# Performance work log

Measured on AMD Instinct MI355X. Metric: run time of the kernel, lower is better.

## Reference

```python
import jax, jax.numpy as jnp
import numpy as np

B, T, C, H = 4, 4096, 512, 64

def setup_inputs() -> dict:
    key = jax.random.key(0)
    ks = jax.random.split(key, 9)
    k = jax.random.normal(ks[0], (B, T, C), dtype=jnp.float32)
    v = jax.random.normal(ks[1], (B, T, C), dtype=jnp.float32)
    q = jax.random.normal(ks[2], (B, T, C), dtype=jnp.float32)
    # causal lower-triangular mask, positions with 0 are masked to -inf
    mask = jnp.tril(jnp.ones((T, T), dtype=jnp.int32))
    s = 1.0 / np.sqrt(C)
    kW = jax.random.normal(ks[3], (C, H), dtype=jnp.float32) * s
    kb = jax.random.normal(ks[4], (H,), dtype=jnp.float32) * s
    vW = jax.random.normal(ks[5], (C, H), dtype=jnp.float32) * s
    vb = jax.random.normal(ks[6], (H,), dtype=jnp.float32) * s
    qW = jax.random.normal(ks[7], (C, H), dtype=jnp.float32) * s
    qb = jax.random.normal(ks[8], (H,), dtype=jnp.float32) * s
    return {"k": k, "v": v, "q": q, "mask": mask,
            "kW": kW, "kb": kb, "vW": vW, "vb": vb, "qW": qW, "qb": qb}

def reference(k, v, q, mask, kW, kb, vW, vb, qW, qb):
    C_in = k.shape[-1]
    kp = k @ kW + kb                              # [B,T,H]
    qp = q @ qW + qb                              # [B,T,H]
    # NOTE: original scales by embedding_size**-0.5 (C), not head_size**-0.5
    attn = jnp.einsum('bth,bsh->bts', qp, kp) * (C_in ** -0.5)  # [B,T,T]
    attn = jnp.where(mask[None, :, :] == 0, -jnp.inf, attn)
    attn = jax.nn.softmax(attn, axis=-1)
    vp = v @ vW + vb                              # [B,T,H]
    out = attn @ vp                               # [B,T,H]
    return out
```

## Files before the change

### kernel.cpp

```cpp
#include <hip/hip_runtime.h>
#include <hip/hip_bf16.h>

#define Bq 4
#define Tq 4096
#define Cq 512
#define Hq 64
#define NEG_BIG (-3.0e38f)

using bf16   = __bf16;
using bf16x8 = __attribute__((ext_vector_type(8))) __bf16;
using bf16x4 = __attribute__((ext_vector_type(4))) __bf16;
using f32x4  = __attribute__((ext_vector_type(4))) float;
using f32x16 = __attribute__((ext_vector_type(16))) float;

static __device__ __forceinline__ float other_half_f(float x) {
    return __shfl_xor(x, 32, 64);
}
static __device__ __forceinline__ unsigned other_half_u(unsigned x) {
    return (unsigned)__shfl_xor((int)x, 32, 64);
}
static __device__ __forceinline__ unsigned pk2(float x, float y) {
    union { bf16 h[2]; unsigned u; } t;
    t.h[0] = (bf16)x; t.h[1] = (bf16)y;
    return t.u;
}
union W8 { unsigned u[4]; bf16x8 v; };

#define BUILD_B(p, BA, BB) do {                                                \
    const unsigned w0 = pk2(p[0],  p[1]),  w1 = pk2(p[2],  p[3]);              \
    const unsigned w2 = pk2(p[4],  p[5]),  w3 = pk2(p[6],  p[7]);              \
    const unsigned w4 = pk2(p[8],  p[9]),  w5 = pk2(p[10], p[11]);             \
    const unsigned w6 = pk2(p[12], p[13]), w7 = pk2(p[14], p[15]);             \
    const unsigned o0 = other_half_u(w0), o1 = other_half_u(w1);               \
    const unsigned o2 = other_half_u(w2), o3 = other_half_u(w3);               \
    const unsigned o4 = other_half_u(w4), o5 = other_half_u(w5);               \
    const unsigned o6 = other_half_u(w6), o7 = other_half_u(w7);               \
    BA.u[0] = hi ? o2 : w0;  BA.u[1] = hi ? o3 : w1;                           \
    BA.u[2] = hi ? w2 : o0;  BA.u[3] = hi ? w3 : o1;                           \
    BB.u[0] = hi ? o6 : w4;  BB.u[1] = hi ? o7 : w5;                           \
    BB.u[2] = hi ? w6 : o4;  BB.u[3] = hi ? w7 : o5;                           \
} while (0)

__global__ __launch_bounds__(256) void prep_weights_kernel(
    const float* __restrict__ kW, const float* __restrict__ qW,
    const float* __restrict__ vW, bf16* __restrict__ WT)
{
    int i = blockIdx.x * 256 + threadIdx.x;
    int t = i >> 15;
    int r = i & 32767;
    int c = r >> 6;
    int h = r & 63;
    const float* W = (t == 0) ? kW : (t == 1) ? qW : vW;
    WT[(size_t)t * 32768 + h * 512 + c] = (bf16)W[r];
}

__global__ __launch_bounds__(128) void proj_kernel(
    const float* __restrict__ Xk, const float* __restrict__ Xq,
    const float* __restrict__ Xv, const bf16* __restrict__ WT,
    const float* __restrict__ bk, const float* __restrict__ bq,
    const float* __restrict__ bv,
    bf16* __restrict__ kp, bf16* __restrict__ qp, bf16* __restrict__ vpT)
{
    const int t    = blockIdx.y;
    const int lane = threadIdx.x & 63;
    const int wave = threadIdx.x >> 6;
    const int lq   = lane & 15;
    const int lg   = lane >> 4;
    const int row0 = blockIdx.x * 32 + wave * 16;

    const float* X    = (t == 0) ? Xk : (t == 1) ? Xq : Xv;
    const float* bias = (t == 0) ? bk : (t == 1) ? bq : bv;
    const bf16*  Wt   = WT + (size_t)t * (Hq * Cq);

    const float* Xrow = X + (size_t)(row0 + lq) * Cq + lg * 8;

    f32x4 acc[4];
#pragma unroll
    for (int i = 0; i < 4; ++i) acc[i] = f32x4{0.f, 0.f, 0.f, 0.f};

#pragma unroll 4
    for (int kc = 0; kc < Cq; kc += 32) {
        float4 a0 = *(const float4*)(Xrow + kc);
        float4 a1 = *(const float4*)(Xrow + kc + 4);
        bf16x8 af;
        af[0] = (bf16)a0.x; af[1] = (bf16)a0.y; af[2] = (bf16)a0.z; af[3] = (bf16)a0.w;
        af[4] = (bf16)a1.x; af[5] = (bf16)a1.y; af[6] = (bf16)a1.z; af[7] = (bf16)a1.w;
#pragma unroll
        for (int ht = 0; ht < 4; ++ht) {
            bf16x8 bfB = *(const bf16x8*)(Wt + (size_t)(ht * 16 + lq) * Cq + kc + lg * 8);
            acc[ht] = __builtin_amdgcn_mfma_f32_16x16x32_bf16(af, bfB, acc[ht], 0, 0, 0);
        }
    }

    const float scale = (t == 1) ? (0.044194173824159216f * 1.4426950408889634f) : 1.0f;

    if (t < 2) {
        bf16* dst = (t == 0) ? kp : qp;
#pragma unroll
        for (int ht = 0; ht < 4; ++ht) {
            float bb = bias[ht * 16 + lq];
#pragma unroll
            for (int r = 0; r < 4; ++r) {
                int row = row0 + 4 * lg + r;
                dst[(size_t)row * Hq + ht * 16 + lq] = (bf16)((acc[ht][r] + bb) * scale);
            }
        }
    } else {
#pragma unroll
        for (int ht = 0; ht < 4; ++ht) {
            float bb = bias[ht * 16 + lq];
            bf16x4 pk;
#pragma unroll
            for (int r = 0; r < 4; ++r) pk[r] = (bf16)(acc[ht][r] + bb);
            int rowg = row0 + 4 * lg;
            int bidx = rowg >> 12;
            int tt   = rowg & 4095;
            int h    = ht * 16 + lq;
            *(bf16x4*)(vpT + (((size_t)(bidx * Hq + h)) << 12) + tt) = pk;
        }
    }
}

__global__ __launch_bounds__(256, 2) void attn_kernel(
    const bf16* __restrict__ qp, const bf16* __restrict__ kp,
    const bf16* __restrict__ vpT,
    bf16* __restrict__ PO, float* __restrict__ PML)
{
    __shared__ char lds_raw[2][16384];

    const int x = blockIdx.x;
    const int b = x & 3;
    const int j = 31 - ((x >> 2) & 31);
    const int c = x >> 7;
    const int kstart = c * 512;
    const int klim   = (j + 1) * 128;
    if (kstart >= klim) return;
    const int kend = min(kstart + 512, klim);
    const int nt   = (kend - kstart) >> 6;

    const int tid  = threadIdx.x;
    const int wid  = tid >> 6;
    const int lane = tid & 63;
    const int l31  = lane & 31;
    const int half = lane >> 5;
    const bool hi  = half != 0;
    const int qt   = j * 4 + wid;
    const int qb   = qt * 32;
    const int qg   = qb + l31;
    const int qlast = qb + 31;

    const bf16* kp_b = kp  + (size_t)b * Tq * Hq;
    const bf16* vp_b = vpT + (size_t)b * Hq * Tq;

    const int srow = tid >> 2;
    const int sseg = (tid & 3) * 16;
    const int sswz = (srow & 7) << 4;

#define STAGE_LOAD(T, r0, r1, r2, r3) do {                                     \
    const int k0_ = kstart + (T) * 64;                                         \
    const bf16* kg_ = kp_b + (size_t)(k0_ + srow) * Hq + (sseg >> 1);          \
    r0 = *(const int4*)(kg_);                                                  \
    r1 = *(const int4*)(kg_ + 32);                                             \
    const bf16* vg_ = vp_b + (size_t)srow * Tq + k0_ + (sseg >> 1);            \
    r2 = *(const int4*)(vg_);                                                  \
    r3 = *(const int4*)(vg_ + 32);                                             \
} while (0)

#define STAGE_WRITE(BUF, r0, r1, r2, r3) do {                                  \
    char* base_ = lds_raw[BUF];                                                \
    *(int4*)(base_ + srow * 128 + (sseg ^ sswz))          = r0;                \
    *(int4*)(base_ + srow * 128 + ((sseg + 64) ^ sswz))   = r1;                \
    *(int4*)(base_ + 8192 + srow * 128 + (sseg ^ sswz))        = r2;           \
    *(int4*)(base_ + 8192 + srow * 128 + ((sseg + 64) ^ sswz)) = r3;           \
} while (0)

    const bf16* qrow = qp + ((size_t)b * Tq + qb + l31) * Hq + half * 8;
    const bf16x8 Q0 = *(const bf16x8*)(qrow);
    const bf16x8 Q1 = *(const bf16x8*)(qrow + 16);
    const bf16x8 Q2 = *(const bf16x8*)(qrow + 32);
    const bf16x8 Q3 = *(const bf16x8*)(qrow + 48);

    f32x16 O0, O1;
#pragma unroll
    for (int r = 0; r < 16; ++r) { O0[r] = 0.f; O1[r] = 0.f; }
    float l = 0.f;

    const int rswz = (l31 & 7) << 4;
    const int cb   = half * 16;

    int4 s0, s1, s2, s3;
    STAGE_LOAD(0, s0, s1, s2, s3);
    STAGE_WRITE(0, s0, s1, s2, s3);
    __syncthreads();

    int cur = 0;
    for (int t = 0; t < nt; ++t) {
        const bool more = (t + 1 < nt);
        if (more) STAGE_LOAD(t + 1, s0, s1, s2, s3);

        const int k0t = kstart + t * 64;
        if (k0t <= qlast) {
            const char* base = lds_raw[cur];
            const char* kr0 = base + l31 * 128;
            const char* kr1 = base + (32 + l31) * 128;
            const char* vr0 = base + 8192 + l31 * 128;
            const char* vr1 = base + 8192 + (32 + l31) * 128;

            const bf16x8 K00 = *(const bf16x8*)(kr0 + ((cb +  0) ^ rswz));
            const bf16x8 K01 = *(const bf16x8*)(kr0 + ((cb + 32) ^ rswz));
            const bf16x8 K02 = *(const bf16x8*)(kr0 + ((cb + 64) ^ rswz));
            const bf16x8 K03 = *(const bf16x8*)(kr0 + ((cb + 96) ^ rswz));
            const bf16x8 K10 = *(const bf16x8*)(kr1 + ((cb +  0) ^ rswz));
            const bf16x8 K11 = *(const bf16x8*)(kr1 + ((cb + 32) ^ rswz));
            const bf16x8 K12 = *(const bf16x8*)(kr1 + ((cb + 64) ^ rswz));
            const bf16x8 K13 = *(const bf16x8*)(kr1 + ((cb + 96) ^ rswz));
            const bf16x8 Vh0k0 = *(const bf16x8*)(vr0 + ((cb +  0) ^ rswz));
            const bf16x8 Vh0k1 = *(const bf16x8*)(vr0 + ((cb + 32) ^ rswz));
            const bf16x8 Vh0k2 = *(const bf16x8*)(vr0 + ((cb + 64) ^ rswz));
            const bf16x8 Vh0k3 = *(const bf16x8*)(vr0 + ((cb + 96) ^ rswz));
            const bf16x8 Vh1k0 = *(const bf16x8*)(vr1 + ((cb +  0) ^ rswz));
            const bf16x8 Vh1k1 = *(const bf16x8*)(vr1 + ((cb + 32) ^ rswz));
            const bf16x8 Vh1k2 = *(const bf16x8*)(vr1 + ((cb + 64) ^ rswz));
            const bf16x8 Vh1k3 = *(const bf16x8*)(vr1 + ((cb + 96) ^ rswz));

            f32x16 S0, S1;
#pragma unroll
            for (int r = 0; r < 16; ++r) { S0[r] = 0.f; S1[r] = 0.f; }
            S0 = __builtin_amdgcn_mfma_f32_32x32x16_bf16(K00, Q0, S0, 0, 0, 0);
            S1 = __builtin_amdgcn_mfma_f32_32x32x16_bf16(K10, Q0, S1, 0, 0, 0);
            S0 = __builtin_amdgcn_mfma_f32_32x32x16_bf16(K01, Q1, S0, 0, 0, 0);
            S1 = __builtin_amdgcn_mfma_f32_32x32x16_bf16(K11, Q1, S1, 0, 0, 0);
            S0 = __builtin_amdgcn_mfma_f32_32x32x16_bf16(K02, Q2, S0, 0, 0, 0);
            S1 = __builtin_amdgcn_mfma_f32_32x32x16_bf16(K12, Q2, S1, 0, 0, 0);
            S0 = __builtin_amdgcn_mfma_f32_32x32x16_bf16(K03, Q3, S0, 0, 0, 0);
            S1 = __builtin_amdgcn_mfma_f32_32x32x16_bf16(K13, Q3, S1, 0, 0, 0);

            if (k0t + 63 > qb) {
#pragma unroll
                for (int r = 0; r < 16; ++r) {
                    const int kg = k0t + (r & 3) + 8 * (r >> 2) + 4 * half;
                    if (kg > qg)      S0[r] = NEG_BIG;
                    if (kg + 32 > qg) S1[r] = NEG_BIG;
                }
            }

            float p0[16], p1[16];
#pragma unroll
            for (int r = 0; r < 16; ++r) {
                p0[r] = exp2f(S0[r]);
                p1[r] = exp2f(S1[r]);
            }
            l += (((p0[0]+p0[1])+(p0[2]+p0[3])) + ((p0[4]+p0[5])+(p0[6]+p0[7])))
               + (((p0[8]+p0[9])+(p0[10]+p0[11])) + ((p0[12]+p0[13])+(p0[14]+p0[15])))
               + (((p1[0]+p1[1])+(p1[2]+p1[3])) + ((p1[4]+p1[5])+(p1[6]+p1[7])))
               + (((p1[8]+p1[9])+(p1[10]+p1[11])) + ((p1[12]+p1[13])+(p1[14]+p1[15])));

            W8 B00, B01, B10, B11;
            BUILD_B(p0, B00, B01);
            BUILD_B(p1, B10, B11);

            O0 = __builtin_amdgcn_mfma_f32_32x32x16_bf16(Vh0k0, B00.v, O0, 0, 0, 0);
            O1 = __builtin_amdgcn_mfma_f32_32x32x16_bf16(Vh1k0, B00.v, O1, 0, 0, 0);
            O0 = __builtin_amdgcn_mfma_f32_32x32x16_bf16(Vh0k1, B01.v, O0, 0, 0, 0);
            O1 = __builtin_amdgcn_mfma_f32_32x32x16_bf16(Vh1k1, B01.v, O1, 0, 0, 0);
            O0 = __builtin_amdgcn_mfma_f32_32x32x16_bf16(Vh0k2, B10.v, O0, 0, 0, 0);
            O1 = __builtin_amdgcn_mfma_f32_32x32x16_bf16(Vh1k2, B10.v, O1, 0, 0, 0);
            O0 = __builtin_amdgcn_mfma_f32_32x32x16_bf16(Vh0k3, B11.v, O0, 0, 0, 0);
            O1 = __builtin_amdgcn_mfma_f32_32x32x16_bf16(Vh1k3, B11.v, O1, 0, 0, 0);
        }

        __syncthreads();
        if (more) STAGE_WRITE(cur ^ 1, s0, s1, s2, s3);
        __syncthreads();
        cur ^= 1;
    }
#undef STAGE_LOAD
#undef STAGE_WRITE

    const float ltot = l + other_half_f(l);
    const float inv  = (ltot > 0.f) ? (1.0f / ltot) : 0.f;
    const size_t slot = ((size_t)(b * 128 + qt)) * 8 + c;
    bf16* po = PO + slot * 2048;
#pragma unroll
    for (int r = 0; r < 16; ++r) {
        const int h = (r & 3) + 8 * (r >> 2) + 4 * half;
        po[h * 32 + l31]        = (bf16)(O0[r] * inv);
        po[(h + 32) * 32 + l31] = (bf16)(O1[r] * inv);
    }
    if (lane < 32) {
        PML[slot * 32 + l31] = ltot;
    }
}

__global__ __launch_bounds__(256) void combine_kernel(
    const bf16* __restrict__ PO, const float* __restrict__ PML,
    float* __restrict__ out)
{
    const int gid = blockIdx.x;
    const int b   = gid & 3;
    const int qt  = gid >> 2;
    const int qb  = qt * 32;
    const int nch = ((qt >> 2) + 4) >> 2;
    const size_t slot0 = ((size_t)(b * 128 + qt)) * 8;
    const int tid = threadIdx.x;
    const int q   = tid & 31;
    const int hh  = tid >> 5;

    float L = 0.f;
    float acc[8];
#pragma unroll
    for (int i = 0; i < 8; ++i) acc[i] = 0.f;

    for (int c = 0; c < nch; ++c) {
        const float w = PML[(slot0 + c) * 32 + q];
        L += w;
        const bf16* po = PO + (slot0 + c) * 2048;
#pragma unroll
        for (int ih = 0; ih < 8; ++ih)
            acc[ih] += w * (float)po[(hh + 8 * ih) * 32 + q];
    }
    const float inv = 1.0f / L;
#pragma unroll
    for (int ih = 0; ih < 8; ++ih)
        out[((size_t)b * Tq + qb + q) * Hq + hh + 8 * ih] = acc[ih] * inv;
}

extern "C" void kernel_launch(void* const* d_in, const int* in_sizes, int n_in,
                              void* d_out, int out_size, void* d_ws, size_t ws_size,
                              hipStream_t stream)
{
    const float* k  = (const float*)d_in[0];
    const float* v  = (const float*)d_in[1];
    const float* q  = (const float*)d_in[2];
    const float* kW = (const float*)d_in[4];
    const float* kb = (const float*)d_in[5];
    const float* vW = (const float*)d_in[6];
    const float* vb = (const float*)d_in[7];
    const float* qW = (const float*)d_in[8];
    const float* qb = (const float*)d_in[9];
    float* out = (float*)d_out;

    char* ws = (char*)d_ws;
    bf16*  WT  = (bf16*)(ws);
    bf16*  kp  = (bf16*)(ws + 196608);
    bf16*  qp  = (bf16*)(ws + 196608 + 2097152);
    bf16*  vpT = (bf16*)(ws + 196608 + 2 * 2097152);
    bf16*  PO  = (bf16*)(ws + 196608 + 3 * 2097152);
    float* PML = (float*)(ws + 196608 + 3 * 2097152 + 16777216);

    hipLaunchKernelGGL(prep_weights_kernel, dim3(384), dim3(256), 0, stream,
                       kW, qW, vW, WT);
    hipLaunchKernelGGL(proj_kernel, dim3(512, 3), dim3(128), 0, stream,
                       k, q, v, WT, kb, qb, vb, kp, qp, vpT);
    hipLaunchKernelGGL(attn_kernel, dim3(1024), dim3(256), 0, stream,
                       qp, kp, vpT, PO, PML);
    hipLaunchKernelGGL(combine_kernel, dim3(512), dim3(256), 0, stream,
                       PO, PML, out);
}
```

Baseline: 82.67 us.

## Stage projection inputs into LDS via async global_load_lds with swizzled double buffer

The projection kernel now runs one wave per 16-row block. Each block streams its full 16x512 fp32 input tile into LDS as two halves, using direct global-to-LDS 16-byte loads with an XOR swizzle. The first half's MFMA work starts while the second half is still in flight, and row reads are fully coalesced instead of strided 32-byte per-lane reads. The trade-off is 32KB of LDS per single-wave block, which limits how many waves can reside on each CU.

New measurement: 84.43 us. 2.1% more time.

```diff
diff --git a/kernel.cpp b/kernel.cpp
--- a/kernel.cpp
+++ b/kernel.cpp
@@ -54,43 +54,89 @@
     WT[(size_t)t * 32768 + h * 512 + c] = (bf16)W[r];
 }
 
-__global__ __launch_bounds__(128) void proj_kernel(
+__global__ __launch_bounds__(64) void proj_kernel(
     const float* __restrict__ Xk, const float* __restrict__ Xq,
     const float* __restrict__ Xv, const bf16* __restrict__ WT,
     const float* __restrict__ bk, const float* __restrict__ bq,
     const float* __restrict__ bv,
     bf16* __restrict__ kp, bf16* __restrict__ qp, bf16* __restrict__ vpT)
 {
-    const int t    = blockIdx.y;
-    const int lane = threadIdx.x & 63;
-    const int wave = threadIdx.x >> 6;
-    const int lq   = lane & 15;
-    const int lg   = lane >> 4;
-    const int row0 = blockIdx.x * 32 + wave * 16;
-
+    __shared__ float Xs[2][16 * 256];
+
+    const int t = blockIdx.y;
     const float* X    = (t == 0) ? Xk : (t == 1) ? Xq : Xv;
     const float* bias = (t == 0) ? bk : (t == 1) ? bq : bv;
     const bf16*  Wt   = WT + (size_t)t * (Hq * Cq);
 
-    const float* Xrow = X + (size_t)(row0 + lq) * Cq + lg * 8;
+    const int lane = threadIdx.x;
+    const int lq   = lane & 15;
+    const int lg   = lane >> 4;
+    const int row0 = blockIdx.x * 16;
+    const float* Xb = X + (size_t)row0 * Cq;
+
+#define STAGE(BUF, HALF) do {                                                  \
+    _Pragma("unroll")                                                          \
+    for (int i = 0; i < 16; ++i) {                                             \
+        const float* src_ = Xb + (size_t)i * Cq + (HALF) * 256                 \
+                          + ((lane ^ (i & 7)) << 2);                           \
+        __builtin_amdgcn_global_load_lds(                                      \
+            (const __attribute__((address_space(1))) void*)(src_),             \
+            (__attribute__((address_space(3))) void*)(&Xs[BUF][i * 256]),      \
+            16, 0, 0);                                                         \
+    }                                                                          \
+} while (0)
+
+    STAGE(0, 0);
+    __builtin_amdgcn_sched_barrier(0);
+    STAGE(1, 1);
+    __builtin_amdgcn_sched_barrier(0);
 
     f32x4 acc[4];
 #pragma unroll
     for (int i = 0; i < 4; ++i) acc[i] = f32x4{0.f, 0.f, 0.f, 0.f};
 
-#pragma unroll 4
-    for (int kc = 0; kc < Cq; kc += 32) {
-        float4 a0 = *(const float4*)(Xrow + kc);
-        float4 a1 = *(const float4*)(Xrow + kc + 4);
+    const int rx = lq & 7;
+    const float* lrow0 = &Xs[0][lq * 256];
+    const float* lrow1 = &Xs[1][lq * 256];
+
+    asm volatile("s_waitcnt vmcnt(16)" ::: "memory");
+    __builtin_amdgcn_sched_barrier(0);
+
+#pragma unroll
+    for (int st = 0; st < 8; ++st) {
+        const int u0 = st * 8 + lg * 2;
+        const float4 x0 = *(const float4*)(lrow0 + (((u0)     ^ rx) << 2));
+        const float4 x1 = *(const float4*)(lrow0 + (((u0 + 1) ^ rx) << 2));
         bf16x8 af;
-        af[0] = (bf16)a0.x; af[1] = (bf16)a0.y; af[2] = (bf16)a0.z; af[3] = (bf16)a0.w;
-        af[4] = (bf16)a1.x; af[5] = (bf16)a1.y; af[6] = (bf16)a1.z; af[7] = (bf16)a1.w;
+        af[0] = (bf16)x0.x; af[1] = (bf16)x0.y; af[2] = (bf16)x0.z; af[3] = (bf16)x0.w;
+        af[4] = (bf16)x1.x; af[5] = (bf16)x1.y; af[6] = (bf16)x1.z; af[7] = (bf16)x1.w;
+        const int kg = st * 32;
 #pragma unroll
         for (int ht = 0; ht < 4; ++ht) {
-            bf16x8 bfB = *(const bf16x8*)(Wt + (size_t)(ht * 16 + lq) * Cq + kc + lg * 8);
+            bf16x8 bfB = *(const bf16x8*)(Wt + (size_t)(ht * 16 + lq) * Cq + kg + lg * 8);
             acc[ht] = __builtin_amdgcn_mfma_f32_16x16x32_bf16(af, bfB, acc[ht], 0, 0, 0);
         }
     }
+
+    asm volatile("s_waitcnt vmcnt(0)" ::: "memory");
+    __builtin_amdgcn_sched_barrier(0);
+
+#pragma unroll
+    for (int st = 0; st < 8; ++st) {
+        const int u0 = st * 8 + lg * 2;
+        const float4 x0 = *(const float4*)(lrow1 + (((u0)     ^ rx) << 2));
+        const float4 x1 = *(const float4*)(lrow1 + (((u0 + 1) ^ rx) << 2));
+        bf16x8 af;
+        af[0] = (bf16)x0.x; af[1] = (bf16)x0.y; af[2] = (bf16)x0.z; af[3] = (bf16)x0.w;
+        af[4] = (bf16)x1.x; af[5] = (bf16)x1.y; af[6] = (bf16)x1.z; af[7] = (bf16)x1.w;
+        const int kg = 256 + st * 32;
+#pragma unroll
+        for (int ht = 0; ht < 4; ++ht) {
+            bf16x8 bfB = *(const bf16x8*)(Wt + (size_t)(ht * 16 + lq) * Cq + kg + lg * 8);
+            acc[ht] = __builtin_amdgcn_mfma_f32_16x16x32_bf16(af, bfB, acc[ht], 0, 0, 0);
+        }
+    }
+#undef STAGE
 
     const float scale = (t == 1) ? (0.044194173824159216f * 1.4426950408889634f) : 1.0f;
 
@@ -350,7 +396,7 @@
 
     hipLaunchKernelGGL(prep_weights_kernel, dim3(384), dim3(256), 0, stream,
                        kW, qW, vW, WT);
-    hipLaunchKernelGGL(proj_kernel, dim3(512, 3), dim3(128), 0, stream,
+    hipLaunchKernelGGL(proj_kernel, dim3(1024, 3), dim3(64), 0, stream,
                        k, q, v, WT, kb, qb, vb, kp, qp, vpT);
     hipLaunchKernelGGL(attn_kernel, dim3(1024), dim3(256), 0, stream,
                        qp, kp, vpT, PO, PML);
```
